# Performance work log

Measured on AMD Instinct MI355X. Metric: run time of the kernel, lower is better.

Reference implementation:

```python
import jax, jax.numpy as jnp
import numpy as np
import math

# cfg constants (YOLOv3/v5 style): strides per feature level, anchors per level
LEN_W = [8.0, 16.0, 32.0]
LEN_H = [8.0, 16.0, 32.0]
ANCHORS = np.array([[[10., 13.], [16., 30.], [33., 23.]],
                    [[30., 61.], [62., 45.], [59., 119.]],
                    [[116., 90.], [156., 198.], [373., 326.]]], dtype=np.float32)
W_OBJ, W_NOOBJ, W_BOX, W_SEG = 1.0, 10.0, 3.0, 2.0


def bce_logits(x, z):
    # numerically stable BCEWithLogits, elementwise
    return jnp.maximum(x, 0.0) - x * z + jnp.log1p(jnp.exp(-jnp.abs(x)))


def ciou_xywh(b1, b2, eps=1e-7):
    # b1, b2: [N,4] (cx, cy, w, h); CIoU as in YOLOv5 bbox_iou(..., CIoU=True)
    b1x1, b1x2 = b1[:, 0] - b1[:, 2] / 2, b1[:, 0] + b1[:, 2] / 2
    b1y1, b1y2 = b1[:, 1] - b1[:, 3] / 2, b1[:, 1] + b1[:, 3] / 2
    b2x1, b2x2 = b2[:, 0] - b2[:, 2] / 2, b2[:, 0] + b2[:, 2] / 2
    b2y1, b2y2 = b2[:, 1] - b2[:, 3] / 2, b2[:, 1] + b2[:, 3] / 2
    inter = jnp.clip(jnp.minimum(b1x2, b2x2) - jnp.maximum(b1x1, b2x1), 0) * \
            jnp.clip(jnp.minimum(b1y2, b2y2) - jnp.maximum(b1y1, b2y1), 0)
    w1, h1 = b1x2 - b1x1, b1y2 - b1y1 + eps
    w2, h2 = b2x2 - b2x1, b2y2 - b2y1 + eps
    union = w1 * h1 + w2 * h2 - inter + eps
    iou = inter / union
    cw = jnp.maximum(b1x2, b2x2) - jnp.minimum(b1x1, b2x1)
    ch = jnp.maximum(b1y2, b2y2) - jnp.minimum(b1y1, b2y1)
    c2 = cw ** 2 + ch ** 2 + eps
    rho2 = ((b2x1 + b2x2 - b1x1 - b1x2) ** 2 + (b2y1 + b2y2 - b1y1 - b1y2) ** 2) / 4
    v = (4.0 / math.pi ** 2) * (jnp.arctan(w2 / h2) - jnp.arctan(w1 / h1)) ** 2
    alpha = jax.lax.stop_gradient(v / (v - iou + (1.0 + eps)))
    return iou - (rho2 / c2 + v * alpha)


def iou_xyxy(b1, b2):
    # faithful to iou_one2one: box2 interpreted as (x1,y1,x2,y2), no eps
    ix1 = jnp.maximum(b1[:, 0], b2[:, 0]); iy1 = jnp.maximum(b1[:, 1], b2[:, 1])
    ix2 = jnp.minimum(b1[:, 2], b2[:, 2]); iy2 = jnp.minimum(b1[:, 3], b2[:, 3])
    inter = jnp.clip(ix2 - ix1, 0.0) * jnp.clip(iy2 - iy1, 0.0)
    a1 = (b1[:, 2] - b1[:, 0]) * (b1[:, 3] - b1[:, 1])
    a2 = (b2[:, 2] - b2[:, 0]) * (b2[:, 3] - b2[:, 1])
    return inter / (a1 + a2 - inter)


def setup_inputs() -> dict:
    key = jax.random.key(0)
    ks = jax.random.split(key, 8)
    B, A, H, W, CH = 16, 3, 80, 80, 85
    N, SEGC, SH, SW = 4096, 21, 160, 160
    prd_f = jax.random.normal(ks[0], (B, A, H, W, CH), jnp.float32) * 0.5
    # target: ch0 misc, ch1:5 = gt box (x1,y1,x2,y2 valid), ch5:9 misc, ch9 = class idx
    x1 = jax.random.uniform(ks[1], (B, A, H, W, 1)) * 600.0
    y1 = jax.random.uniform(ks[2], (B, A, H, W, 1)) * 600.0
    wh = jax.random.uniform(ks[3], (B, A, H, W, 2)) * 40.0 + 2.0
    c0 = jax.random.uniform(ks[4], (B, A, H, W, 1))
    mid = jax.random.uniform(ks[5], (B, A, H, W, 4))
    cls = jax.random.randint(ks[6], (B, A, H, W, 1), 0, 80).astype(jnp.float32)
    target_f = jnp.concatenate([c0, x1, y1, x1 + wh[..., 0:1], y1 + wh[..., 1:2], mid, cls], axis=-1)
    flat = jax.random.permutation(ks[7], B * A * H * W)[:N]  # unique positive cells
    indices_f = jnp.stack(jnp.unravel_index(flat, (B, A, H, W)), 0).astype(jnp.int32)
    seg = jax.random.normal(jax.random.fold_in(key, 10), (B, SEGC, SH, SW), jnp.float32)
    seg_label = jax.random.randint(jax.random.fold_in(key, 11), (B, SH, SW), 0, SEGC)
    return {"prd_f": prd_f, "target_f": target_f, "indices_f": indices_f,
            "f_idx": 0, "seg": seg, "seg_label": seg_label}


def reference(prd_f, target_f, indices_f, f_idx, seg, seg_label):
    anchors = jnp.asarray(ANCHORS)[f_idx]            # [3,2]
    lw, lh = LEN_W[f_idx], LEN_H[f_idx]
    b, a, h, w = indices_f[0], indices_f[1], indices_f[2], indices_f[3]
    ps = prd_f[b, a, h, w]                           # [N, 5+C]
    sxy = jax.nn.sigmoid(ps[:, 0:2])                 # in-place sigmoid in original
    fdt = prd_f.dtype
    px = lw * (sxy[:, 0] + w.astype(fdt))
    py = lh * (sxy[:, 1] + h.astype(fdt))
    pcw = anchors[a, 0] * jnp.exp(ps[:, 2])
    pch = anchors[a, 1] * jnp.exp(ps[:, 3])
    pbox = jnp.stack([px, py, pcw, pch], axis=1)     # [N,4] cxcywh
    ts = target_f[b, a, h, w, 1:5]                   # [N,4] gt boxes
    lbox = (1.0 - ciou_xywh(pbox, ts)).mean()
    # --- gt_map path (detached in original) ---
    pb = jax.lax.stop_gradient(pbox)
    pxyxy = jnp.stack([pb[:, 0] - pb[:, 2] / 2, pb[:, 1] - pb[:, 3] / 2,
                       pb[:, 0] + pb[:, 2] / 2, pb[:, 1] + pb[:, 3] / 2], axis=1)
    one_iou = jax.lax.stop_gradient(iou_xyxy(pxyxy, ts))  # gt_map[...,5] at positives
    B, A, H, W, _ = prd_f.shape
    obj = jnp.zeros((B, A, H, W), bool).at[b, a, h, w].set(True)
    obj_logit = prd_f[..., 4]
    # lobj: BCE at positive cells (targets = per-cell IoU)
    lobj = bce_logits(ps[:, 4], one_iou).mean()
    # lnoobj: BCE at negative cells (targets = 0)
    noobj = ~obj
    lnoobj = jnp.sum(jnp.where(noobj, bce_logits(obj_logit, 0.0), 0.0)) / jnp.sum(noobj)
    # lcls: CE at positive cells, labels from target_f[...,9]
    labels = target_f[b, a, h, w, 9].astype(jnp.int32)
    logp = jax.nn.log_softmax(ps[:, 5:], axis=-1)
    lcls = -jnp.mean(jnp.take_along_axis(logp, labels[:, None], axis=1))
    # lseg: CE over channel dim of seg
    seg_logp = jax.nn.log_softmax(seg, axis=1)
    lseg = -jnp.mean(jnp.take_along_axis(seg_logp, seg_label[:, None, :, :], axis=1))
    return W_BOX * lbox + W_OBJ * lobj + W_NOOBJ * lnoobj + lcls + W_SEG * lseg
```

## Files before the change

kernel.cpp:

```cpp
#include <hip/hip_runtime.h>
#include <math.h>

#define BB   16
#define AA   3
#define HHH  80
#define WWW  80
#define CHN  85
#define TCH  10
#define SEGC 21
#define SH   160
#define SW   160
#define PTOT (BB*AA*HHH*WWW)
#define SPIX (BB*SH*SW)
#define PIX_PER_IMG (SH*SW)
#define F4_PER_IMG (PIX_PER_IMG/4)

#define NB_NOOBJ 300
#define NB_SEG   400
#define NB_OBJ   512
#define NB_TOTAL (NB_NOOBJ + NB_SEG + NB_OBJ)

#define OFF_NOOBJ 0
#define OFF_SEG   300
#define OFF_OBJ   700

__constant__ float c_anchors[3][3][2] = {
  {{10.f,13.f},{16.f,30.f},{33.f,23.f}},
  {{30.f,61.f},{62.f,45.f},{59.f,119.f}},
  {{116.f,90.f},{156.f,198.f},{373.f,326.f}}
};
__constant__ float c_len[3] = {8.f, 16.f, 32.f};

__device__ inline float softplusf(float x) {
  return fmaxf(x, 0.f) + log1pf(expf(-fabsf(x)));
}

__device__ inline double block_reduce(double v) {
  #pragma unroll
  for (int off = 32; off; off >>= 1) v += __shfl_xor(v, off, 64);
  __shared__ double sm[4];
  int lane = threadIdx.x & 63, wid = threadIdx.x >> 6;
  if (lane == 0) sm[wid] = v;
  __syncthreads();
  return (threadIdx.x == 0) ? (sm[0] + sm[1] + sm[2] + sm[3]) : 0.0;
}

__global__ void __launch_bounds__(256) k_fused(
    const float* __restrict__ prd, const float* __restrict__ tgt,
    const int* __restrict__ ind, const int* __restrict__ fidx,
    const float* __restrict__ seg, const int* __restrict__ lab,
    double* __restrict__ ws, int N) {
  const int t = threadIdx.x;
  const int blk = blockIdx.x;

  if (blk < NB_NOOBJ) {
    int base = blk * 1024 + t;
    float x0 = prd[(size_t)(base       ) * CHN + 4];
    float x1 = prd[(size_t)(base + 256 ) * CHN + 4];
    float x2 = prd[(size_t)(base + 512 ) * CHN + 4];
    float x3 = prd[(size_t)(base + 768 ) * CHN + 4];
    float s = softplusf(x0) + softplusf(x1) + softplusf(x2) + softplusf(x3);
    double tot = block_reduce((double)s);
    if (t == 0) ws[OFF_NOOBJ + blk] = tot;
  } else if (blk < NB_NOOBJ + NB_SEG) {
    int g4 = (blk - NB_NOOBJ) * 256 + t;
    int bimg = g4 / F4_PER_IMG;
    int r4 = g4 - bimg * F4_PER_IMG;
    const float4* sp = (const float4*)(seg + (size_t)bimg * SEGC * PIX_PER_IMG) + r4;
    int4 L = ((const int4*)lab)[g4];
    float sx = 0.f, sy = 0.f, sz = 0.f, sw = 0.f;
    float lx = 0.f, ly = 0.f, lz = 0.f, lw = 0.f;
    #pragma unroll
    for (int c = 0; c < SEGC; ++c) {
      float4 v = sp[(size_t)c * F4_PER_IMG];
      sx += expf(v.x); sy += expf(v.y); sz += expf(v.z); sw += expf(v.w);
      if (c == L.x) lx = v.x;
      if (c == L.y) ly = v.y;
      if (c == L.z) lz = v.z;
      if (c == L.w) lw = v.w;
    }
    float loss = (logf(sx) - lx) + (logf(sy) - ly) + (logf(sz) - lz) + (logf(sw) - lw);
    double tot = block_reduce((double)loss);
    if (t == 0) ws[OFF_SEG + (blk - NB_NOOBJ)] = tot;
  } else {
    const int bc = blk - NB_NOOBJ - NB_SEG;
    const int wv = t >> 6, ln = t & 63;
    const int f = fidx[0];
    const float lwc = c_len[f], lhc = c_len[f];
    const float eps = 1e-7f;
    double lbox = 0, lobj = 0, lcls = 0, osp = 0;

    for (int obj = bc * 4 + wv; obj < N; obj += NB_OBJ * 4) {
      int b  = ind[obj];
      int a  = ind[N + obj];
      int hh = ind[2*N + obj];
      int ww = ind[3*N + obj];
      size_t cell  = (((size_t)b*AA + a)*HHH + hh)*WWW + ww;
      size_t pbase = cell * CHN;
      size_t tbase = cell * TCH;

      float v0 = prd[pbase + ln];
      float v1 = (ln < CHN - 64) ? prd[pbase + 64 + ln] : 0.f;
      float ts0 = tgt[tbase+1], ts1 = tgt[tbase+2], ts2 = tgt[tbase+3], ts3 = tgt[tbase+4];
      int lab2 = (int)tgt[tbase+9];

      float a0 = (ln >= 5) ? v0 : -INFINITY;
      float a1 = (ln < CHN - 64) ? v1 : -INFINITY;
      float m = fmaxf(a0, a1);
      #pragma unroll
      for (int off = 32; off; off >>= 1) m = fmaxf(m, __shfl_xor(m, off, 64));
      float s = ((ln >= 5) ? expf(a0 - m) : 0.f) + ((ln < CHN - 64) ? expf(a1 - m) : 0.f);
      #pragma unroll
      for (int off = 32; off; off >>= 1) s += __shfl_xor(s, off, 64);
      float lse = m + logf(s);

      float ps0 = __shfl(v0, 0, 64), ps1 = __shfl(v0, 1, 64), ps2 = __shfl(v0, 2, 64),
            ps3 = __shfl(v0, 3, 64), ps4 = __shfl(v0, 4, 64);
      int ci = 5 + lab2;
      float psl = (ci < 64) ? __shfl(v0, ci, 64) : __shfl(v1, ci - 64, 64);

      float sxg = 1.f/(1.f + expf(-ps0)), syg = 1.f/(1.f + expf(-ps1));
      float px = lwc*(sxg + (float)ww), py = lhc*(syg + (float)hh);
      float pcw = c_anchors[f][a][0]*expf(ps2);
      float pch = c_anchors[f][a][1]*expf(ps3);

      float b1x1 = px - pcw*0.5f, b1x2 = px + pcw*0.5f;
      float b1y1 = py - pch*0.5f, b1y2 = py + pch*0.5f;
      float b2x1 = ts0 - ts2*0.5f, b2x2 = ts0 + ts2*0.5f;
      float b2y1 = ts1 - ts3*0.5f, b2y2 = ts1 + ts3*0.5f;
      float iw = fminf(b1x2,b2x2) - fmaxf(b1x1,b2x1);
      float ih = fminf(b1y2,b2y2) - fmaxf(b1y1,b2y1);
      float inter = fmaxf(iw,0.f)*fmaxf(ih,0.f);
      float w1 = b1x2-b1x1, h1 = b1y2-b1y1+eps;
      float w2 = b2x2-b2x1, h2 = b2y2-b2y1+eps;
      float uni = w1*h1 + w2*h2 - inter + eps;
      float iou = inter/uni;
      float cwv = fmaxf(b1x2,b2x2) - fminf(b1x1,b2x1);
      float chv = fmaxf(b1y2,b2y2) - fminf(b1y1,b2y1);
      float c2 = cwv*cwv + chv*chv + eps;
      float dxv = b2x1+b2x2-b1x1-b1x2, dyv = b2y1+b2y2-b1y1-b1y2;
      float rho2 = (dxv*dxv + dyv*dyv)*0.25f;
      float da = atanf(w2/h2) - atanf(w1/h1);
      float vterm = (4.f/(float)(M_PI*M_PI)) * da * da;
      float alpha = vterm/(vterm - iou + 1.f + eps);
      float ciou = iou - (rho2/c2 + vterm*alpha);
      lbox += (double)(1.f - ciou);

      float ix1 = fmaxf(b1x1, ts0), iy1 = fmaxf(b1y1, ts1);
      float ix2 = fminf(b1x2, ts2), iy2 = fminf(b1y2, ts3);
      float inter2 = fmaxf(ix2-ix1,0.f)*fmaxf(iy2-iy1,0.f);
      float a1r = (b1x2-b1x1)*(b1y2-b1y1);
      float a2r = (ts2-ts0)*(ts3-ts1);
      float one_iou = inter2/(a1r + a2r - inter2);

      lobj += (double)(fmaxf(ps4,0.f) - ps4*one_iou + log1pf(expf(-fabsf(ps4))));
      lcls += (double)(lse - psl);
      osp  += (double)softplusf(ps4);
    }

    __shared__ double ssum[4][4];
    if (ln == 0) {
      ssum[wv][0] = lbox; ssum[wv][1] = lobj; ssum[wv][2] = lcls; ssum[wv][3] = osp;
    }
    __syncthreads();
    if (t < 4) {
      double v = ssum[0][t] + ssum[1][t] + ssum[2][t] + ssum[3][t];
      ws[OFF_OBJ + (size_t)bc * 4 + t] = v;
    }
  }
}

__global__ void __launch_bounds__(256) k_final(const double* __restrict__ ws,
                                               float* __restrict__ out, int N) {
  const int t = threadIdx.x;
  double sn = 0, ss = 0, s0 = 0, s1 = 0, s2 = 0, s3 = 0;
  for (int i = t; i < NB_NOOBJ; i += 256) sn += ws[OFF_NOOBJ + i];
  for (int i = t; i < NB_SEG;   i += 256) ss += ws[OFF_SEG + i];
  for (int i = t; i < NB_OBJ;   i += 256) {
    const double* r = ws + OFF_OBJ + (size_t)i * 4;
    s0 += r[0]; s1 += r[1]; s2 += r[2]; s3 += r[3];
  }
  double comp[6] = {s0, s1, s2, s3, sn, ss};
  __shared__ double red[6][4];
  #pragma unroll
  for (int c = 0; c < 6; ++c) {
    double v = comp[c];
    #pragma unroll
    for (int off = 32; off; off >>= 1) v += __shfl_xor(v, off, 64);
    if ((t & 63) == 0) red[c][t >> 6] = v;
  }
  __syncthreads();
  if (t == 0) {
    double P[6];
    #pragma unroll
    for (int c = 0; c < 6; ++c) P[c] = red[c][0]+red[c][1]+red[c][2]+red[c][3];
    double lnoobj = (P[4] - P[3]) / (double)(PTOT - N);
    out[0] = (float)(3.0*(P[0]/N) + (P[1]/N) + 10.0*lnoobj + (P[2]/N)
                     + 2.0*(P[5]/(double)SPIX));
  }
}

extern "C" void kernel_launch(void* const* d_in, const int* in_sizes, int n_in,
                              void* d_out, int out_size, void* d_ws, size_t ws_size,
                              hipStream_t stream) {
  const float* prd  = (const float*)d_in[0];
  const float* tgt  = (const float*)d_in[1];
  const int*   ind  = (const int*)d_in[2];
  const int*   fidx = (const int*)d_in[3];
  const float* seg  = (const float*)d_in[4];
  const int*   slab = (const int*)d_in[5];
  float* out = (float*)d_out;
  double* ws = (double*)d_ws;
  int N = in_sizes[2] / 4;

  k_fused<<<NB_TOTAL, 256, 0, stream>>>(prd, tgt, ind, fidx, seg, slab, ws, N);
  k_final<<<1,        256, 0, stream>>>(ws, out, N);
}
```

Baseline: 182.9 us.

## Use fast exp/log intrinsics and spread noobj reduction over more blocks

```diff
diff --git a/kernel.cpp b/kernel.cpp
--- a/kernel.cpp
+++ b/kernel.cpp
@@ -15,14 +15,14 @@
 #define PIX_PER_IMG (SH*SW)
 #define F4_PER_IMG (PIX_PER_IMG/4)
 
-#define NB_NOOBJ 300
+#define NB_NOOBJ 1200
 #define NB_SEG   400
 #define NB_OBJ   512
 #define NB_TOTAL (NB_NOOBJ + NB_SEG + NB_OBJ)
 
 #define OFF_NOOBJ 0
-#define OFF_SEG   300
-#define OFF_OBJ   700
+#define OFF_SEG   1200
+#define OFF_OBJ   1600
 
 __constant__ float c_anchors[3][3][2] = {
   {{10.f,13.f},{16.f,30.f},{33.f,23.f}},
@@ -31,8 +31,8 @@
 };
 __constant__ float c_len[3] = {8.f, 16.f, 32.f};
 
-__device__ inline float softplusf(float x) {
-  return fmaxf(x, 0.f) + log1pf(expf(-fabsf(x)));
+__device__ inline float softplus_fast(float x) {
+  return fmaxf(x, 0.f) + __logf(1.f + __expf(-fabsf(x)));
 }
 
 __device__ inline double block_reduce(double v) {
@@ -45,7 +45,7 @@
   return (threadIdx.x == 0) ? (sm[0] + sm[1] + sm[2] + sm[3]) : 0.0;
 }
 
-__global__ void __launch_bounds__(256) k_fused(
+__global__ void __launch_bounds__(256, 4) k_fused(
     const float* __restrict__ prd, const float* __restrict__ tgt,
     const int* __restrict__ ind, const int* __restrict__ fidx,
     const float* __restrict__ seg, const int* __restrict__ lab,
@@ -54,13 +54,9 @@
   const int blk = blockIdx.x;
 
   if (blk < NB_NOOBJ) {
-    int base = blk * 1024 + t;
-    float x0 = prd[(size_t)(base       ) * CHN + 4];
-    float x1 = prd[(size_t)(base + 256 ) * CHN + 4];
-    float x2 = prd[(size_t)(base + 512 ) * CHN + 4];
-    float x3 = prd[(size_t)(base + 768 ) * CHN + 4];
-    float s = softplusf(x0) + softplusf(x1) + softplusf(x2) + softplusf(x3);
-    double tot = block_reduce((double)s);
+    int cell = blk * 256 + t;
+    float x = prd[(size_t)cell * CHN + 4];
+    double tot = block_reduce((double)softplus_fast(x));
     if (t == 0) ws[OFF_NOOBJ + blk] = tot;
   } else if (blk < NB_NOOBJ + NB_SEG) {
     int g4 = (blk - NB_NOOBJ) * 256 + t;
@@ -73,13 +69,14 @@
     #pragma unroll
     for (int c = 0; c < SEGC; ++c) {
       float4 v = sp[(size_t)c * F4_PER_IMG];
-      sx += expf(v.x); sy += expf(v.y); sz += expf(v.z); sw += expf(v.w);
+      sx += __expf(v.x); sy += __expf(v.y); sz += __expf(v.z); sw += __expf(v.w);
       if (c == L.x) lx = v.x;
       if (c == L.y) ly = v.y;
       if (c == L.z) lz = v.z;
       if (c == L.w) lw = v.w;
     }
-    float loss = (logf(sx) - lx) + (logf(sy) - ly) + (logf(sz) - lz) + (logf(sw) - lw);
+    float loss = (__logf(sx) - lx) + (__logf(sy) - ly)
+               + (__logf(sz) - lz) + (__logf(sw) - lw);
     double tot = block_reduce((double)loss);
     if (t == 0) ws[OFF_SEG + (blk - NB_NOOBJ)] = tot;
   } else {
@@ -109,20 +106,20 @@
       float m = fmaxf(a0, a1);
       #pragma unroll
       for (int off = 32; off; off >>= 1) m = fmaxf(m, __shfl_xor(m, off, 64));
-      float s = ((ln >= 5) ? expf(a0 - m) : 0.f) + ((ln < CHN - 64) ? expf(a1 - m) : 0.f);
+      float s = ((ln >= 5) ? __expf(a0 - m) : 0.f) + ((ln < CHN - 64) ? __expf(a1 - m) : 0.f);
       #pragma unroll
       for (int off = 32; off; off >>= 1) s += __shfl_xor(s, off, 64);
-      float lse = m + logf(s);
+      float lse = m + __logf(s);
 
       float ps0 = __shfl(v0, 0, 64), ps1 = __shfl(v0, 1, 64), ps2 = __shfl(v0, 2, 64),
             ps3 = __shfl(v0, 3, 64), ps4 = __shfl(v0, 4, 64);
       int ci = 5 + lab2;
       float psl = (ci < 64) ? __shfl(v0, ci, 64) : __shfl(v1, ci - 64, 64);
 
-      float sxg = 1.f/(1.f + expf(-ps0)), syg = 1.f/(1.f + expf(-ps1));
+      float sxg = 1.f/(1.f + __expf(-ps0)), syg = 1.f/(1.f + __expf(-ps1));
       float px = lwc*(sxg + (float)ww), py = lhc*(syg + (float)hh);
-      float pcw = c_anchors[f][a][0]*expf(ps2);
-      float pch = c_anchors[f][a][1]*expf(ps3);
+      float pcw = c_anchors[f][a][0]*__expf(ps2);
+      float pch = c_anchors[f][a][1]*__expf(ps3);
 
       float b1x1 = px - pcw*0.5f, b1x2 = px + pcw*0.5f;
       float b1y1 = py - pch*0.5f, b1y2 = py + pch*0.5f;
@@ -153,9 +150,9 @@
       float a2r = (ts2-ts0)*(ts3-ts1);
       float one_iou = inter2/(a1r + a2r - inter2);
 
-      lobj += (double)(fmaxf(ps4,0.f) - ps4*one_iou + log1pf(expf(-fabsf(ps4))));
+      lobj += (double)(fmaxf(ps4,0.f) - ps4*one_iou + __logf(1.f + __expf(-fabsf(ps4))));
       lcls += (double)(lse - psl);
-      osp  += (double)softplusf(ps4);
+      osp  += (double)softplus_fast(ps4);
     }
 
     __shared__ double ssum[4][4];
```

Measured after the change: 181.8 us, median of 2. Within noise of the previous version (-0.6%).
